# Performance work log

Measured on AMD Instinct MI355X. Metric: run time of the kernel, lower is better.

Reference implementation:

```python
import jax, jax.numpy as jnp
import numpy as np

STRIDE = 1
PADDING = (1, 1, 1, 1)  # (left, right, top, bottom), as in torch F.pad for last two dims
NEG_INF = -jnp.inf


def maxplus_conv2d(x, kernel, stride=STRIDE):
    """Tropical (max-plus) conv2d, groups=1.
    x: [B, C, H, W] (already padded), kernel: [O, C, kh, kw].
    out[b,o,h,w] = max_{c,ki,kj} x[b,c,h*s+ki,w*s+kj] + kernel[o,c,ki,kj]
    """
    B, C, H, W = x.shape
    O, Cg, kh, kw = kernel.shape
    Ho = (H - kh) // stride + 1
    Wo = (W - kw) // stride + 1
    out = jnp.full((B, O, Ho, Wo), NEG_INF, dtype=x.dtype)
    # Loop over the small, fixed kernel taps (kh*kw = 9); reductions over the
    # channel axis stay fully vectorized and fuse into a single add+reduce-max.
    for ki in range(kh):
        for kj in range(kw):
            xs = x[:, :, ki:ki + Ho * stride:stride, kj:kj + Wo * stride:stride]  # [B,C,Ho,Wo]
            cand = jnp.max(xs[:, None, :, :, :] + kernel[None, :, :, ki, kj][:, :, :, None, None], axis=2)
            out = jnp.maximum(out, cand)
    return out


def setup_inputs() -> dict:
    key = jax.random.key(0)
    kx, kk = jax.random.split(key)
    x = jax.random.normal(kx, (8, 64, 64, 64), dtype=jnp.float32)
    kernel = jax.random.normal(kk, (64, 64, 3, 3), dtype=jnp.float32) * 0.1
    return {"x": x, "kernel": kernel}


def reference(x, kernel):
    left, right, top, bottom = PADDING
    # MaxPlus semifield: pad with the additive identity of max, i.e. -inf
    xp = jnp.pad(x, ((0, 0), (0, 0), (top, bottom), (left, right)), mode="constant", constant_values=NEG_INF)
    return maxplus_conv2d(xp, kernel, STRIDE)
```

## Files before the change

kernel.cpp:

```cpp
#include <hip/hip_runtime.h>

#define NEG_INF (-__builtin_huge_valf())
#define NEG_INF_BITS 0xFF800000

template <int CTRL>
__device__ __forceinline__ float dpp_neighbor(float v) {
    return __int_as_float(__builtin_amdgcn_update_dpp(
        (int)NEG_INF_BITS, __float_as_int(v), CTRL, 0xF, 0xF, false));
}

__device__ __forceinline__ void maxplus9(const float xv[3][6], const float* k9,
                                         float a[4]) {
#pragma unroll
    for (int wi = 0; wi < 4; ++wi) {
        float m = a[wi];
        float t0 = xv[0][wi + 0] + k9[0];
        float t1 = xv[0][wi + 1] + k9[1];
        m = fmaxf(m, fmaxf(t0, t1));
        t0 = xv[0][wi + 2] + k9[2];
        t1 = xv[1][wi + 0] + k9[3];
        m = fmaxf(m, fmaxf(t0, t1));
        t0 = xv[1][wi + 1] + k9[4];
        t1 = xv[1][wi + 2] + k9[5];
        m = fmaxf(m, fmaxf(t0, t1));
        t0 = xv[2][wi + 0] + k9[6];
        t1 = xv[2][wi + 1] + k9[7];
        m = fmaxf(m, fmaxf(t0, t1));
        m = fmaxf(m, xv[2][wi + 2] + k9[8]);
        a[wi] = m;
    }
}

__global__ __launch_bounds__(64, 4)
void maxplus_conv2d_kernel(const float* __restrict__ x,
                           const float* __restrict__ kern,
                           float* __restrict__ out) {
    const int tid = threadIdx.x;
    const int wg  = tid & 15;
    const int hr  = tid >> 4;
    const int w0  = wg << 2;

    const int h_base = blockIdx.x * 4;
    const int b      = blockIdx.y;
    const int o_base = blockIdx.z << 1;

    const float* xb = x + (size_t)b * (64 * 64 * 64);

    int  off[3];
    bool rv[3];
#pragma unroll
    for (int r = 0; r < 3; ++r) {
        int gh = h_base + hr - 1 + r;
        rv[r]  = (unsigned)gh < 64u;
        off[r] = (rv[r] ? gh : 0) * 64 + w0;
    }

    float acc[2][4];
#pragma unroll
    for (int oo = 0; oo < 2; ++oo)
#pragma unroll
        for (int wi = 0; wi < 4; ++wi)
            acc[oo][wi] = NEG_INF;

    const float* kp0 = kern + (size_t)(o_base + 0) * (64 * 9);
    const float* kp1 = kern + (size_t)(o_base + 1) * (64 * 9);

#pragma unroll 1
    for (int cc = 0; cc < 64; cc += 4) {
        float kv[4][2][9];
#pragma unroll
        for (int cl = 0; cl < 4; ++cl)
#pragma unroll
            for (int t = 0; t < 9; ++t) {
                kv[cl][0][t] = kp0[(cc + cl) * 9 + t];
                kv[cl][1][t] = kp1[(cc + cl) * 9 + t];
            }

        float4 mm[4][3];
#pragma unroll
        for (int cl = 0; cl < 4; ++cl)
#pragma unroll
            for (int r = 0; r < 3; ++r)
                mm[cl][r] = *(const float4*)(xb + ((cc + cl) * 4096 + off[r]));

#pragma unroll
        for (int cl = 0; cl < 4; ++cl) {
            float xv[3][6];
#pragma unroll
            for (int r = 0; r < 3; ++r) {
                float4 m = mm[cl][r];
                if (r != 1 && !rv[r])
                    m = make_float4(NEG_INF, NEG_INF, NEG_INF, NEG_INF);
                xv[r][0] = dpp_neighbor<0x111>(m.w);
                xv[r][1] = m.x; xv[r][2] = m.y; xv[r][3] = m.z; xv[r][4] = m.w;
                xv[r][5] = dpp_neighbor<0x101>(m.x);
            }
            maxplus9(xv, kv[cl][0], acc[0]);
            maxplus9(xv, kv[cl][1], acc[1]);
        }
    }

    const int h = h_base + hr;
#pragma unroll
    for (int oo = 0; oo < 2; ++oo) {
        float4 v = make_float4(acc[oo][0], acc[oo][1], acc[oo][2], acc[oo][3]);
        *(float4*)(out + ((((size_t)b * 64 + (o_base + oo)) * 64 + h) * 64 + w0)) = v;
    }
}

extern "C" void kernel_launch(void* const* d_in, const int* in_sizes, int n_in,
                              void* d_out, int out_size, void* d_ws, size_t ws_size,
                              hipStream_t stream) {
    const float* x    = (const float*)d_in[0];
    const float* kern = (const float*)d_in[1];
    float* out = (float*)d_out;

    dim3 grid(16, 8, 32);
    dim3 block(64);
    maxplus_conv2d_kernel<<<grid, block, 0, stream>>>(x, kern, out);
}
```

Measured before the change: 121.1 us.

## Stage kernel weights in LDS, pack two outputs as v2f, double-buffer input loads

Kernel weights for the block's two output channels are staged once into LDS, interleaved as float2 pairs, instead of being reloaded from global memory on every channel step. The accumulators and weight adds use 2-wide float vectors so the compiler can emit packed f32 adds (v_pk_add_f32). Input rows are double-buffered across channel halves to overlap global loads with compute. The cost is an LDS allocation, a block barrier, and more live registers, which may lower occupancy.

New measurement: 260.6 us. +115.3%, slower.

```diff
diff --git a/kernel.cpp b/kernel.cpp
--- a/kernel.cpp
+++ b/kernel.cpp
@@ -1,4 +1,6 @@
 #include <hip/hip_runtime.h>
+
+typedef float v2f __attribute__((ext_vector_type(2)));
 
 #define NEG_INF (-__builtin_huge_valf())
 #define NEG_INF_BITS 0xFF800000
@@ -9,32 +11,62 @@
         (int)NEG_INF_BITS, __float_as_int(v), CTRL, 0xF, 0xF, false));
 }
 
-__device__ __forceinline__ void maxplus9(const float xv[3][6], const float* k9,
-                                         float a[4]) {
-#pragma unroll
-    for (int wi = 0; wi < 4; ++wi) {
-        float m = a[wi];
-        float t0 = xv[0][wi + 0] + k9[0];
-        float t1 = xv[0][wi + 1] + k9[1];
-        m = fmaxf(m, fmaxf(t0, t1));
-        t0 = xv[0][wi + 2] + k9[2];
-        t1 = xv[1][wi + 0] + k9[3];
-        m = fmaxf(m, fmaxf(t0, t1));
-        t0 = xv[1][wi + 1] + k9[4];
-        t1 = xv[1][wi + 2] + k9[5];
-        m = fmaxf(m, fmaxf(t0, t1));
-        t0 = xv[2][wi + 0] + k9[6];
-        t1 = xv[2][wi + 1] + k9[7];
-        m = fmaxf(m, fmaxf(t0, t1));
-        m = fmaxf(m, xv[2][wi + 2] + k9[8]);
-        a[wi] = m;
-    }
+__device__ __forceinline__ v2f vmax2(v2f a, v2f b) {
+    v2f r; r.x = fmaxf(a.x, b.x); r.y = fmaxf(a.y, b.y); return r;
 }
+
+#define LOADH(DST, CC, CL0)                                                   \
+    do {                                                                      \
+        _Pragma("unroll") for (int q = 0; q < 2; ++q)                         \
+            _Pragma("unroll") for (int r = 0; r < 3; ++r)                     \
+                DST[q][r] = *(const float4*)(xb + (((CC) + (CL0) + q) * 4096  \
+                                                   + off[r]));                \
+    } while (0)
+
+#define COMP(SRC, CC, CL0)                                                    \
+    do {                                                                      \
+        _Pragma("unroll") for (int q = 0; q < 2; ++q) {                       \
+            const v2f* kq = &kls[((CC) + (CL0) + q) * 9];                     \
+            v2f kk[9];                                                        \
+            _Pragma("unroll") for (int t = 0; t < 9; ++t) kk[t] = kq[t];      \
+            float xv[3][6];                                                   \
+            _Pragma("unroll") for (int r = 0; r < 3; ++r) {                   \
+                float4 m = SRC[q][r];                                         \
+                if (r != 1 && !rv[r])                                         \
+                    m = make_float4(NEG_INF, NEG_INF, NEG_INF, NEG_INF);      \
+                xv[r][0] = dpp_neighbor<0x111>(m.w);                          \
+                xv[r][1] = m.x; xv[r][2] = m.y;                               \
+                xv[r][3] = m.z; xv[r][4] = m.w;                               \
+                xv[r][5] = dpp_neighbor<0x101>(m.x);                          \
+            }                                                                 \
+            _Pragma("unroll") for (int wi = 0; wi < 4; ++wi) {                \
+                v2f m = acc2[wi];                                             \
+                v2f t0, t1;                                                   \
+                t0 = (v2f){xv[0][wi + 0], xv[0][wi + 0]} + kk[0];             \
+                t1 = (v2f){xv[0][wi + 1], xv[0][wi + 1]} + kk[1];             \
+                m = vmax2(m, vmax2(t0, t1));                                  \
+                t0 = (v2f){xv[0][wi + 2], xv[0][wi + 2]} + kk[2];             \
+                t1 = (v2f){xv[1][wi + 0], xv[1][wi + 0]} + kk[3];             \
+                m = vmax2(m, vmax2(t0, t1));                                  \
+                t0 = (v2f){xv[1][wi + 1], xv[1][wi + 1]} + kk[4];             \
+                t1 = (v2f){xv[1][wi + 2], xv[1][wi + 2]} + kk[5];             \
+                m = vmax2(m, vmax2(t0, t1));                                  \
+                t0 = (v2f){xv[2][wi + 0], xv[2][wi + 0]} + kk[6];             \
+                t1 = (v2f){xv[2][wi + 1], xv[2][wi + 1]} + kk[7];             \
+                m = vmax2(m, vmax2(t0, t1));                                  \
+                t0 = (v2f){xv[2][wi + 2], xv[2][wi + 2]} + kk[8];             \
+                m = vmax2(m, t0);                                             \
+                acc2[wi] = m;                                                 \
+            }                                                                 \
+        }                                                                     \
+    } while (0)
 
 __global__ __launch_bounds__(64, 4)
 void maxplus_conv2d_kernel(const float* __restrict__ x,
                            const float* __restrict__ kern,
                            float* __restrict__ out) {
+    __shared__ v2f kls[64 * 9];
+
     const int tid = threadIdx.x;
     const int wg  = tid & 15;
     const int hr  = tid >> 4;
@@ -43,6 +75,17 @@
     const int h_base = blockIdx.x * 4;
     const int b      = blockIdx.y;
     const int o_base = blockIdx.z << 1;
+
+    {
+        const float* k0p = kern + (size_t)(o_base + 0) * 576;
+        const float* k1p = kern + (size_t)(o_base + 1) * 576;
+#pragma unroll
+        for (int i = 0; i < 9; ++i) {
+            int idx = i * 64 + tid;
+            kls[idx] = (v2f){k0p[idx], k1p[idx]};
+        }
+    }
+    __syncthreads();
 
     const float* xb = x + (size_t)b * (64 * 64 * 64);
 
@@ -55,57 +98,27 @@
         off[r] = (rv[r] ? gh : 0) * 64 + w0;
     }
 
-    float acc[2][4];
+    v2f acc2[4];
 #pragma unroll
-    for (int oo = 0; oo < 2; ++oo)
-#pragma unroll
-        for (int wi = 0; wi < 4; ++wi)
-            acc[oo][wi] = NEG_INF;
+    for (int wi = 0; wi < 4; ++wi) acc2[wi] = (v2f){NEG_INF, NEG_INF};
 
-    const float* kp0 = kern + (size_t)(o_base + 0) * (64 * 9);
-    const float* kp1 = kern + (size_t)(o_base + 1) * (64 * 9);
+    float4 A[2][3], B2[2][3];
+    LOADH(A, 0, 0);
 
 #pragma unroll 1
     for (int cc = 0; cc < 64; cc += 4) {
-        float kv[4][2][9];
-#pragma unroll
-        for (int cl = 0; cl < 4; ++cl)
-#pragma unroll
-            for (int t = 0; t < 9; ++t) {
-                kv[cl][0][t] = kp0[(cc + cl) * 9 + t];
-                kv[cl][1][t] = kp1[(cc + cl) * 9 + t];
-            }
-
-        float4 mm[4][3];
-#pragma unroll
-        for (int cl = 0; cl < 4; ++cl)
-#pragma unroll
-            for (int r = 0; r < 3; ++r)
-                mm[cl][r] = *(const float4*)(xb + ((cc + cl) * 4096 + off[r]));
-
-#pragma unroll
-        for (int cl = 0; cl < 4; ++cl) {
-            float xv[3][6];
-#pragma unroll
-            for (int r = 0; r < 3; ++r) {
-                float4 m = mm[cl][r];
-                if (r != 1 && !rv[r])
-                    m = make_float4(NEG_INF, NEG_INF, NEG_INF, NEG_INF);
-                xv[r][0] = dpp_neighbor<0x111>(m.w);
-                xv[r][1] = m.x; xv[r][2] = m.y; xv[r][3] = m.z; xv[r][4] = m.w;
-                xv[r][5] = dpp_neighbor<0x101>(m.x);
-            }
-            maxplus9(xv, kv[cl][0], acc[0]);
-            maxplus9(xv, kv[cl][1], acc[1]);
-        }
+        LOADH(B2, cc, 2);
+        COMP(A, cc, 0);
+        if (cc + 4 < 64)
+            LOADH(A, cc + 4, 0);
+        COMP(B2, cc, 2);
     }
 
     const int h = h_base + hr;
-#pragma unroll
-    for (int oo = 0; oo < 2; ++oo) {
-        float4 v = make_float4(acc[oo][0], acc[oo][1], acc[oo][2], acc[oo][3]);
-        *(float4*)(out + ((((size_t)b * 64 + (o_base + oo)) * 64 + h) * 64 + w0)) = v;
-    }
+    float4 v0 = make_float4(acc2[0].x, acc2[1].x, acc2[2].x, acc2[3].x);
+    float4 v1 = make_float4(acc2[0].y, acc2[1].y, acc2[2].y, acc2[3].y);
+    *(float4*)(out + ((((size_t)b * 64 + (o_base + 0)) * 64 + h) * 64 + w0)) = v0;
+    *(float4*)(out + ((((size_t)b * 64 + (o_base + 1)) * 64 + h) * 64 + w0)) = v1;
 }
 
 extern "C" void kernel_launch(void* const* d_in, const int* in_sizes, int n_in,
```
